# Kernel tuning notes

Measured on AMD Instinct MI355X. Metric: run time of the kernel, lower is better.

The kernel has to match this reference:

```python
import jax, jax.numpy as jnp
import numpy as np

N = 20          # n_qubits
L = 4           # n_layers
B = 4           # batch of states
DIM = 1 << N    # 2^N = 1048576

_H = jnp.asarray((1.0 / np.sqrt(2.0)) * np.array([[1.0, 1.0], [1.0, -1.0]]), dtype=jnp.complex64)


def _apply_1q(psi, U, q):
    # psi: [B, 2^N]; apply 2x2 unitary U on big-endian qubit q
    left = 1 << q
    right = 1 << (N - q - 1)
    out = jnp.einsum('uv,blvr->blur', U, psi.reshape(-1, left, 2, right))
    return out.reshape(-1, DIM)


def _apply_cnot(psi, control, target):
    ctrl_mask = np.uint32(1 << (N - 1 - control))
    targ_mask = np.uint32(1 << (N - 1 - target))
    idx = jnp.arange(DIM, dtype=jnp.uint32)
    perm = jnp.where((idx & ctrl_mask) != 0, idx ^ targ_mask, idx)
    return psi[:, perm]


def _rot_x(theta):
    c = jnp.cos(theta / 2.0).astype(jnp.complex64)
    s = (-1j * jnp.sin(theta / 2.0)).astype(jnp.complex64)
    return jnp.stack([jnp.stack([c, s]), jnp.stack([s, c])])


def _rot_z(theta):
    e = jnp.exp(-0.5j * theta.astype(jnp.complex64))
    z = jnp.zeros((), jnp.complex64)
    return jnp.stack([jnp.stack([e, z]), jnp.stack([z, jnp.conj(e)])])


def _circuit(psi, thetas_x, thetas_z):
    for q in range(N):
        psi = _apply_1q(psi, _H, q)
    for l in range(L):
        for q in range(N):
            psi = _apply_1q(psi, _rot_z(thetas_z[l, q]), q)
        for q in range(N):
            psi = _apply_1q(psi, _rot_x(thetas_x[l, q]), q)
        for q in range(N - 1):  # linear entanglement
            psi = _apply_cnot(psi, q, q + 1)
    return psi


def setup_inputs() -> dict:
    key = jax.random.key(0)
    k1, k2, k3, k4 = jax.random.split(key, 4)
    return {
        'psi0_real': jax.random.normal(k1, (B, DIM), dtype=jnp.float32),
        'psi0_imag': jax.random.normal(k2, (B, DIM), dtype=jnp.float32),
        'thetas_x': jax.random.normal(k3, (L, N), dtype=jnp.float32),
        'thetas_z': jax.random.normal(k4, (L, N), dtype=jnp.float32),
    }


def reference(psi0_real, psi0_imag, thetas_x, thetas_z):
    psi = (psi0_real + 1j * psi0_imag).astype(jnp.complex64)
    return _circuit(psi, thetas_x, thetas_z)
```

## Files before the change

kernel.cpp:

```cpp
#include <hip/hip_runtime.h>
#include <math.h>


#define NQ 20

struct U2 { float r00,i00,r01,i01,r10,i10,r11,i11; };

typedef unsigned int u32x4 __attribute__((ext_vector_type(4)));
typedef float        f32x4 __attribute__((ext_vector_type(4)));

__device__ __forceinline__ uint4 ld_nt4(const uint4* p) {
  u32x4 v = __builtin_nontemporal_load((const u32x4*)p);
  uint4 r; r.x = v[0]; r.y = v[1]; r.z = v[2]; r.w = v[3]; return r;
}
__device__ __forceinline__ void st_nt4(uint4* p, uint4 v) {
  u32x4 t; t[0] = v.x; t[1] = v.y; t[2] = v.z; t[3] = v.w;
  __builtin_nontemporal_store(t, (u32x4*)p);
}
__device__ __forceinline__ float4 ldf_nt4(const float* p) {
  f32x4 v = __builtin_nontemporal_load((const f32x4*)p);
  return make_float4(v[0], v[1], v[2], v[3]);
}
__device__ __forceinline__ void stf_nt4(float* p, float4 v) {
  f32x4 t; t[0] = v.x; t[1] = v.y; t[2] = v.z; t[3] = v.w;
  __builtin_nontemporal_store(t, (f32x4*)p);
}

__device__ __forceinline__ U2 make_u(const float* __restrict__ thx,
                                     const float* __restrict__ thz,
                                     int layer, int q, int withH) {
  float tx = 0.5f * thx[layer*NQ + q];
  float tz = 0.5f * thz[layer*NQ + q];
  float sx, cxv; __sincosf(tx, &sx, &cxv);
  float sz, cz;  __sincosf(tz, &sz, &cz);
  U2 u;
  u.r00 =  cxv*cz;  u.i00 = -cxv*sz;
  u.r01 =  sx*sz;   u.i01 = -sx*cz;
  u.r10 = -sx*sz;   u.i10 = -sx*cz;
  u.r11 =  cxv*cz;  u.i11 =  cxv*sz;
  if (withH) {
    const float r = 0.70710678118654752f;
    float a, b;
    a=u.r00; b=u.r01; u.r00=(a+b)*r; u.r01=(a-b)*r;
    a=u.i00; b=u.i01; u.i00=(a+b)*r; u.i01=(a-b)*r;
    a=u.r10; b=u.r11; u.r10=(a+b)*r; u.r11=(a-b)*r;
    a=u.i10; b=u.i11; u.i10=(a+b)*r; u.i11=(a-b)*r;
  }
  return u;
}

template <int ST>
__device__ __forceinline__ void bfly16(float* re, float* im, const U2 u) {
#pragma unroll
  for (int s = 0; s < 16; ++s) {
    if ((s & ST) == 0) {
      const int s1 = s + ST;
      float ar = re[s], ai = im[s], br = re[s1], bi = im[s1];
      re[s]  = u.r00*ar - u.i00*ai + u.r01*br - u.i01*bi;
      im[s]  = u.r00*ai + u.i00*ar + u.r01*bi + u.i01*br;
      re[s1] = u.r10*ar - u.i10*ai + u.r11*br - u.i11*bi;
      im[s1] = u.r10*ai + u.i10*ar + u.r11*bi + u.i11*br;
    }
  }
}

template <int ST>
__device__ __forceinline__ void bfly16_rx(float* re, float* im, float c, float s) {
#pragma unroll
  for (int k = 0; k < 16; ++k) {
    if ((k & ST) == 0) {
      const int k1 = k + ST;
      float ar = re[k], ai = im[k], br = re[k1], bi = im[k1];
      re[k]  = c*ar + s*bi;
      im[k]  = c*ai - s*br;
      re[k1] = c*br + s*ai;
      im[k1] = c*bi - s*ar;
    }
  }
}

template <int RXONLY, int ST>
__device__ __forceinline__ void gate16(float* re, float* im,
                                       const float* __restrict__ thx,
                                       const float* __restrict__ thz,
                                       int layer, int q, int withH) {
  if (RXONLY) {
    float sx, cx; __sincosf(0.5f * thx[layer*NQ + q], &sx, &cx);
    bfly16_rx<ST>(re, im, cx, sx);
  } else {
    bfly16<ST>(re, im, make_u(thx, thz, layer, q, withH));
  }
}

__device__ __forceinline__ int K(int j) { return j ^ (((j >> 6) & 0xF) << 2); }

__device__ __forceinline__ unsigned pkbf(float a, float b) {
  unsigned r;
  asm("v_cvt_pk_bf16_f32 %0, %1, %2" : "=v"(r) : "v"(a), "v"(b));
  return r;
}
__device__ __forceinline__ float blo(unsigned p) { return __uint_as_float(p << 16); }
__device__ __forceinline__ float bhi(unsigned p) { return __uint_as_float(p & 0xFFFF0000u); }

__device__ __forceinline__ void unpack_g(uint4 v, float* re, float* im) {
  re[0]=blo(v.x); re[1]=bhi(v.x); re[2]=blo(v.y); re[3]=bhi(v.y);
  im[0]=blo(v.z); im[1]=bhi(v.z); im[2]=blo(v.w); im[3]=bhi(v.w);
}

template <int FIN, int RXONLY, int PP>
__global__ __launch_bounds__(256, 5) void pass_a(
    const uint4* __restrict__ src, uint4* __restrict__ dst,
    float* __restrict__ outre,
    const float* __restrict__ thx, const float* __restrict__ thz,
    int layer, int withH) {
  __shared__ __align__(16) float sre[4096];
  __shared__ __align__(16) float sim[4096];
  float4* sre4 = (float4*)sre;
  float4* sim4 = (float4*)sim;
  const int t = threadIdx.x;
  const int b = blockIdx.x >> 8;
  const int m = blockIdx.x & 255;
  const size_t base = (((size_t)b) << NQ) | ((size_t)m << 12);
  float re[16], im[16];

#pragma unroll
  for (int hi = 0; hi < 4; ++hi) {
    const int o = (hi << 10) | (t << 2);
    unpack_g(ld_nt4(src + ((base + o) >> 2)), re + 4*hi, im + 4*hi);
  }
  gate16<RXONLY,1>(re, im, thx, thz, layer, 19, withH);
  gate16<RXONLY,2>(re, im, thx, thz, layer, 18, withH);
  gate16<RXONLY,4>(re, im, thx, thz, layer,  9, withH);
  gate16<RXONLY,8>(re, im, thx, thz, layer,  8, withH);

#pragma unroll
  for (int hi = 0; hi < 4; ++hi) {
    int F = K((hi << 10) | (t << 2)) >> 2;
    sre4[F] = make_float4(re[4*hi+0], re[4*hi+1], re[4*hi+2], re[4*hi+3]);
    sim4[F] = make_float4(im[4*hi+0], im[4*hi+1], im[4*hi+2], im[4*hi+3]);
  }
  __syncthreads();

  const int jt2 = (t & 3) | ((t & 0xFC) << 4);
#pragma unroll
  for (int s = 0; s < 16; ++s) {
    int k = K(jt2 | (s << 2));
    re[s] = sre[k]; im[s] = sim[k];
  }
  gate16<RXONLY,1>(re, im, thx, thz, layer, 17, withH);
  gate16<RXONLY,2>(re, im, thx, thz, layer, 16, withH);
  gate16<RXONLY,4>(re, im, thx, thz, layer, 15, withH);
  gate16<RXONLY,8>(re, im, thx, thz, layer, 14, withH);
#pragma unroll
  for (int s = 0; s < 16; ++s) {
    int k = K(jt2 | (s << 2));
    sre[k] = re[s]; sim[k] = im[s];
  }
  __syncthreads();

  const int jt3 = (t & 63) | ((t & 0xC0) << 4);
#pragma unroll
  for (int s = 0; s < 16; ++s) {
    int k = K(jt3 | (s << 6));
    re[s] = sre[k]; im[s] = sim[k];
  }
  gate16<RXONLY,1>(re, im, thx, thz, layer, 13, withH);
  gate16<RXONLY,2>(re, im, thx, thz, layer, 12, withH);
  gate16<RXONLY,4>(re, im, thx, thz, layer, 11, withH);
  gate16<RXONLY,8>(re, im, thx, thz, layer, 10, withH);
#pragma unroll
  for (int s = 0; s < 16; ++s) {
    int k = K(jt3 | (s << 6));
    sre[k] = re[s]; sim[k] = im[s];
  }
  __syncthreads();

  const int c11 = (m & 1) << 11;
#pragma unroll
  for (int hi = 0; hi < 4; ++hi) {
    int y0 = (hi << 10) | (t << 2);
    int x0 = y0 ^ ((y0 >> 1) & 0x7FF) ^ c11;
    int FG = K(x0 & ~3) >> 2;
    float4 vr = sre4[FG], vi = sim4[FG];
    if (x0 & 2) {
      vr = make_float4(vr.z, vr.w, vr.x, vr.y);
      vi = make_float4(vi.z, vi.w, vi.x, vi.y);
    }
    if (FIN) {
      stf_nt4(outre + base + y0, make_float4(vr.x, vr.y, vr.w, vr.z));
    } else {
      uint4 v;
      v.x = pkbf(vr.x, vr.y); v.y = pkbf(vr.w, vr.z);
      v.z = pkbf(vi.x, vi.y); v.w = pkbf(vi.w, vi.z);
      size_t n;
      if (PP) {
        n = (((size_t)b) << NQ) | ((size_t)m << 4)
          | (size_t)((y0 & 15) | ((y0 >> 4) << 12));
      } else {
        n = base + y0;
      }
      st_nt4(dst + (n >> 2), v);
    }
  }
}

template <int INIT, int DIAG, int PP>
__global__ __launch_bounds__(256, 5) void pass_b(
    const float* __restrict__ in_re, const float* __restrict__ in_im,
    const uint4* __restrict__ src, uint4* __restrict__ dst,
    const float* __restrict__ thx, const float* __restrict__ thz,
    int layer, int withH) {
  __shared__ __align__(16) float sre[4096];
  __shared__ __align__(16) float sim[4096];
  float4* sre4 = (float4*)sre;
  float4* sim4 = (float4*)sim;
  const int t = threadIdx.x;
  const int b = blockIdx.x >> 8;
  const int m = blockIdx.x & 255;
  const size_t base = ((size_t)b) << NQ;
  float re[16], im[16];

  float pb = 0.f, dhi1 = 0.f, dhi2 = 0.f, de1 = 0.f, de2 = 0.f;
  if (DIAG) {
    const float* Z = thz + layer*NQ;
    float s0 = 0.f;
#pragma unroll
    for (int q = 0; q < NQ; ++q) s0 += Z[q];
    pb = -0.5f * s0;
#pragma unroll
    for (int k = 0; k < 8; ++k)
      pb += (m & (1 << k)) ? Z[15 - k] : 0.f;
    pb += (t & 1) ? Z[17] : 0.f;
    pb += (t & 2) ? Z[16] : 0.f;
#pragma unroll
    for (int k = 2; k < 8; ++k)
      pb += (t & (1 << k)) ? Z[9 - k] : 0.f;
    dhi1 = Z[1];  dhi2 = Z[0];
    de1  = Z[19]; de2  = Z[18];
  }
  const float dhi[4] = {0.f, dhi1, dhi2, dhi1 + dhi2};
  const float de[4]  = {0.f, de1,  de2,  de1 + de2};

#pragma unroll
  for (int hi = 0; hi < 4; ++hi) {
    int j0q = (hi << 10) | (t << 2);
    if (INIT) {
      int g0 = ((j0q >> 4) << 12) | (m << 4) | (j0q & 15);
      float4 vr = ldf_nt4(in_re + base + g0);
      float4 vi = ldf_nt4(in_im + base + g0);
      re[4*hi+0]=vr.x; re[4*hi+1]=vr.y; re[4*hi+2]=vr.z; re[4*hi+3]=vr.w;
      im[4*hi+0]=vi.x; im[4*hi+1]=vi.y; im[4*hi+2]=vi.z; im[4*hi+3]=vi.w;
    } else if (PP) {
      size_t nB = base | ((size_t)m << 12) | (size_t)j0q;
      unpack_g(ld_nt4(src + (nB >> 2)), re + 4*hi, im + 4*hi);
    } else {
      int g0 = ((j0q >> 4) << 12) | (m << 4) | (j0q & 15);
      unpack_g(ld_nt4(src + ((base + g0) >> 2)), re + 4*hi, im + 4*hi);
    }
    if (DIAG) {
      float bh = pb + dhi[hi];
#pragma unroll
      for (int e = 0; e < 4; ++e) {
        float sn, cs; __sincosf(bh + de[e], &sn, &cs);
        float r0 = re[4*hi+e], i0 = im[4*hi+e];
        re[4*hi+e] = cs*r0 - sn*i0;
        im[4*hi+e] = cs*i0 + sn*r0;
      }
    }
  }
  gate16<DIAG,4>(re, im, thx, thz, layer, 1, withH);
  gate16<DIAG,8>(re, im, thx, thz, layer, 0, withH);

#pragma unroll
  for (int hi = 0; hi < 4; ++hi) {
    int F = K((hi << 10) | (t << 2)) >> 2;
    sre4[F] = make_float4(re[4*hi+0], re[4*hi+1], re[4*hi+2], re[4*hi+3]);
    sim4[F] = make_float4(im[4*hi+0], im[4*hi+1], im[4*hi+2], im[4*hi+3]);
  }
  __syncthreads();

  const int jt2 = (t & 15) | ((t & 0xF0) << 4);
#pragma unroll
  for (int s = 0; s < 16; ++s) {
    int k = K(jt2 | (s << 4));
    re[s] = sre[k]; im[s] = sim[k];
  }
  gate16<DIAG,1>(re, im, thx, thz, layer, 7, withH);
  gate16<DIAG,2>(re, im, thx, thz, layer, 6, withH);
  gate16<DIAG,4>(re, im, thx, thz, layer, 5, withH);
  gate16<DIAG,8>(re, im, thx, thz, layer, 4, withH);
#pragma unroll
  for (int s = 0; s < 16; ++s) {
    int k = K(jt2 | (s << 4));
    sre[k] = re[s]; sim[k] = im[s];
  }
  __syncthreads();

  const int jt3 = ((t & 63) << 2) | ((t & 0xC0) << 4);
#pragma unroll
  for (int sh = 0; sh < 4; ++sh) {
    int FG = K(jt3 | (sh << 8)) >> 2;
    float4 vr = sre4[FG], vi = sim4[FG];
    re[4*sh+0]=vr.x; re[4*sh+1]=vr.y; re[4*sh+2]=vr.z; re[4*sh+3]=vr.w;
    im[4*sh+0]=vi.x; im[4*sh+1]=vi.y; im[4*sh+2]=vi.z; im[4*sh+3]=vi.w;
  }
  gate16<DIAG,4>(re, im, thx, thz, layer, 3, withH);
  gate16<DIAG,8>(re, im, thx, thz, layer, 2, withH);
#pragma unroll
  for (int sh = 0; sh < 4; ++sh) {
    int FG = K(jt3 | (sh << 8)) >> 2;
    sre4[FG] = make_float4(re[4*sh+0], re[4*sh+1], re[4*sh+2], re[4*sh+3]);
    sim4[FG] = make_float4(im[4*sh+0], im[4*sh+1], im[4*sh+2], im[4*sh+3]);
  }
  __syncthreads();

#pragma unroll
  for (int hi = 0; hi < 4; ++hi) {
    int y0 = (hi << 10) | (t << 2);
    int x0 = y0 ^ ((y0 >> 1) & 0x7F0);
    int FG = K(x0) >> 2;
    float4 vr = sre4[FG], vi = sim4[FG];
    int g0 = ((y0 >> 4) << 12) | (m << 4) | (y0 & 15);
    uint4 v;
    v.x = pkbf(vr.x, vr.y); v.y = pkbf(vr.z, vr.w);
    v.z = pkbf(vi.x, vi.y); v.w = pkbf(vi.z, vi.w);
    st_nt4(dst + ((base + g0) >> 2), v);
  }
}

extern "C" void kernel_launch(void* const* d_in, const int* in_sizes, int n_in,
                              void* d_out, int out_size, void* d_ws, size_t ws_size,
                              hipStream_t stream) {
  const float* p_re = (const float*)d_in[0];
  const float* p_im = (const float*)d_in[1];
  const float* thx  = (const float*)d_in[2];
  const float* thz  = (const float*)d_in[3];
  float* outre = (float*)d_out;
  const size_t HALF = (size_t)16 << 20;
  uint4* ws0 = (uint4*)d_ws;
  uint4* ws1 = (uint4*)((char*)d_ws + HALF);

  dim3 grid(1024), blk(256);

  if (ws_size >= 2 * HALF) {
    pass_b<1,0,1><<<grid, blk, 0, stream>>>(p_re, p_im, nullptr, ws0, thx, thz, 0, 1);
    pass_a<0,0,1><<<grid, blk, 0, stream>>>(ws0, ws1, outre, thx, thz, 0, 1);
    for (int l = 1; l < 3; ++l) {
      pass_b<0,1,1><<<grid, blk, 0, stream>>>(nullptr, nullptr, ws1, ws0, thx, thz, l, 0);
      pass_a<0,1,1><<<grid, blk, 0, stream>>>(ws0, ws1, outre, thx, thz, l, 0);
    }
    pass_b<0,1,1><<<grid, blk, 0, stream>>>(nullptr, nullptr, ws1, ws0, thx, thz, 3, 0);
    pass_a<1,1,1><<<grid, blk, 0, stream>>>(ws0, nullptr, outre, thx, thz, 3, 0);
  } else {
    pass_b<1,0,0><<<grid, blk, 0, stream>>>(p_re, p_im, nullptr, ws0, thx, thz, 0, 1);
    pass_a<0,0,0><<<grid, blk, 0, stream>>>(ws0, ws0, outre, thx, thz, 0, 1);
    for (int l = 1; l < 3; ++l) {
      pass_b<0,1,0><<<grid, blk, 0, stream>>>(nullptr, nullptr, ws0, ws0, thx, thz, l, 0);
      pass_a<0,1,0><<<grid, blk, 0, stream>>>(ws0, ws0, outre, thx, thz, l, 0);
    }
    pass_b<0,1,0><<<grid, blk, 0, stream>>>(nullptr, nullptr, ws0, ws0, thx, thz, 3, 0);
    pass_a<1,1,0><<<grid, blk, 0, stream>>>(ws0, nullptr, outre, thx, thz, 3, 0);
  }
}
```

Baseline: 178.8 us.

## Store shared-memory staging as packed bf16 complex pairs and raise occupancy

The separate fp32 real/imag shared arrays are replaced by one array of packed bf16 (re,im) words, which halves LDS per block (32KB to 16KB) and LDS traffic for each transpose stage. Launch bounds go from 5 to 8 blocks per SM to use the freed LDS. The final global store becomes bit shuffles instead of cvt. The cost is extra bf16 rounding at every intermediate shared-memory stage, so accuracy drops, and register pressure rises under the tighter launch bound.

```diff
diff --git a/kernel.cpp b/kernel.cpp
--- a/kernel.cpp
+++ b/kernel.cpp
@@ -107,16 +107,19 @@
   im[0]=blo(v.z); im[1]=bhi(v.z); im[2]=blo(v.w); im[3]=bhi(v.w);
 }
 
+__device__ __forceinline__ unsigned pkpair(float r, float i) { return pkbf(r, i); }
+__device__ __forceinline__ void unpair(unsigned u, float* r, float* i) {
+  *r = blo(u); *i = bhi(u);
+}
+
 template <int FIN, int RXONLY, int PP>
-__global__ __launch_bounds__(256, 5) void pass_a(
+__global__ __launch_bounds__(256, 8) void pass_a(
     const uint4* __restrict__ src, uint4* __restrict__ dst,
     float* __restrict__ outre,
     const float* __restrict__ thx, const float* __restrict__ thz,
     int layer, int withH) {
-  __shared__ __align__(16) float sre[4096];
-  __shared__ __align__(16) float sim[4096];
-  float4* sre4 = (float4*)sre;
-  float4* sim4 = (float4*)sim;
+  __shared__ __align__(16) unsigned spk[4096];
+  uint4* spk4 = (uint4*)spk;
   const int t = threadIdx.x;
   const int b = blockIdx.x >> 8;
   const int m = blockIdx.x & 255;
@@ -136,16 +139,17 @@
 #pragma unroll
   for (int hi = 0; hi < 4; ++hi) {
     int F = K((hi << 10) | (t << 2)) >> 2;
-    sre4[F] = make_float4(re[4*hi+0], re[4*hi+1], re[4*hi+2], re[4*hi+3]);
-    sim4[F] = make_float4(im[4*hi+0], im[4*hi+1], im[4*hi+2], im[4*hi+3]);
+    spk4[F] = make_uint4(pkpair(re[4*hi+0], im[4*hi+0]),
+                         pkpair(re[4*hi+1], im[4*hi+1]),
+                         pkpair(re[4*hi+2], im[4*hi+2]),
+                         pkpair(re[4*hi+3], im[4*hi+3]));
   }
   __syncthreads();
 
   const int jt2 = (t & 3) | ((t & 0xFC) << 4);
 #pragma unroll
   for (int s = 0; s < 16; ++s) {
-    int k = K(jt2 | (s << 2));
-    re[s] = sre[k]; im[s] = sim[k];
+    unpair(spk[K(jt2 | (s << 2))], re + s, im + s);
   }
   gate16<RXONLY,1>(re, im, thx, thz, layer, 17, withH);
   gate16<RXONLY,2>(re, im, thx, thz, layer, 16, withH);
@@ -153,16 +157,14 @@
   gate16<RXONLY,8>(re, im, thx, thz, layer, 14, withH);
 #pragma unroll
   for (int s = 0; s < 16; ++s) {
-    int k = K(jt2 | (s << 2));
-    sre[k] = re[s]; sim[k] = im[s];
+    spk[K(jt2 | (s << 2))] = pkpair(re[s], im[s]);
   }
   __syncthreads();
 
   const int jt3 = (t & 63) | ((t & 0xC0) << 4);
 #pragma unroll
   for (int s = 0; s < 16; ++s) {
-    int k = K(jt3 | (s << 6));
-    re[s] = sre[k]; im[s] = sim[k];
+    unpair(spk[K(jt3 | (s << 6))], re + s, im + s);
   }
   gate16<RXONLY,1>(re, im, thx, thz, layer, 13, withH);
   gate16<RXONLY,2>(re, im, thx, thz, layer, 12, withH);
@@ -170,8 +172,7 @@
   gate16<RXONLY,8>(re, im, thx, thz, layer, 10, withH);
 #pragma unroll
   for (int s = 0; s < 16; ++s) {
-    int k = K(jt3 | (s << 6));
-    sre[k] = re[s]; sim[k] = im[s];
+    spk[K(jt3 | (s << 6))] = pkpair(re[s], im[s]);
   }
   __syncthreads();
 
@@ -181,17 +182,17 @@
     int y0 = (hi << 10) | (t << 2);
     int x0 = y0 ^ ((y0 >> 1) & 0x7FF) ^ c11;
     int FG = K(x0 & ~3) >> 2;
-    float4 vr = sre4[FG], vi = sim4[FG];
-    if (x0 & 2) {
-      vr = make_float4(vr.z, vr.w, vr.x, vr.y);
-      vi = make_float4(vi.z, vi.w, vi.x, vi.y);
-    }
+    uint4 q = spk4[FG];
+    if (x0 & 2) q = make_uint4(q.z, q.w, q.x, q.y);
     if (FIN) {
-      stf_nt4(outre + base + y0, make_float4(vr.x, vr.y, vr.w, vr.z));
+      stf_nt4(outre + base + y0,
+              make_float4(blo(q.x), blo(q.y), blo(q.w), blo(q.z)));
     } else {
       uint4 v;
-      v.x = pkbf(vr.x, vr.y); v.y = pkbf(vr.w, vr.z);
-      v.z = pkbf(vi.x, vi.y); v.w = pkbf(vi.w, vi.z);
+      v.x = (q.x & 0xFFFFu) | (q.y << 16);
+      v.y = (q.w & 0xFFFFu) | (q.z << 16);
+      v.z = (q.x >> 16) | (q.y & 0xFFFF0000u);
+      v.w = (q.w >> 16) | (q.z & 0xFFFF0000u);
       size_t n;
       if (PP) {
         n = (((size_t)b) << NQ) | ((size_t)m << 4)
@@ -205,15 +206,13 @@
 }
 
 template <int INIT, int DIAG, int PP>
-__global__ __launch_bounds__(256, 5) void pass_b(
+__global__ __launch_bounds__(256, 8) void pass_b(
     const float* __restrict__ in_re, const float* __restrict__ in_im,
     const uint4* __restrict__ src, uint4* __restrict__ dst,
     const float* __restrict__ thx, const float* __restrict__ thz,
     int layer, int withH) {
-  __shared__ __align__(16) float sre[4096];
-  __shared__ __align__(16) float sim[4096];
-  float4* sre4 = (float4*)sre;
-  float4* sim4 = (float4*)sim;
+  __shared__ __align__(16) unsigned spk[4096];
+  uint4* spk4 = (uint4*)spk;
   const int t = threadIdx.x;
   const int b = blockIdx.x >> 8;
   const int m = blockIdx.x & 255;
@@ -274,16 +273,17 @@
 #pragma unroll
   for (int hi = 0; hi < 4; ++hi) {
     int F = K((hi << 10) | (t << 2)) >> 2;
-    sre4[F] = make_float4(re[4*hi+0], re[4*hi+1], re[4*hi+2], re[4*hi+3]);
-    sim4[F] = make_float4(im[4*hi+0], im[4*hi+1], im[4*hi+2], im[4*hi+3]);
+    spk4[F] = make_uint4(pkpair(re[4*hi+0], im[4*hi+0]),
+                         pkpair(re[4*hi+1], im[4*hi+1]),
+                         pkpair(re[4*hi+2], im[4*hi+2]),
+                         pkpair(re[4*hi+3], im[4*hi+3]));
   }
   __syncthreads();
 
   const int jt2 = (t & 15) | ((t & 0xF0) << 4);
 #pragma unroll
   for (int s = 0; s < 16; ++s) {
-    int k = K(jt2 | (s << 4));
-    re[s] = sre[k]; im[s] = sim[k];
+    unpair(spk[K(jt2 | (s << 4))], re + s, im + s);
   }
   gate16<DIAG,1>(re, im, thx, thz, layer, 7, withH);
   gate16<DIAG,2>(re, im, thx, thz, layer, 6, withH);
@@ -291,8 +291,7 @@
   gate16<DIAG,8>(re, im, thx, thz, layer, 4, withH);
 #pragma unroll
   for (int s = 0; s < 16; ++s) {
-    int k = K(jt2 | (s << 4));
-    sre[k] = re[s]; sim[k] = im[s];
+    spk[K(jt2 | (s << 4))] = pkpair(re[s], im[s]);
   }
   __syncthreads();
 
@@ -300,17 +299,21 @@
 #pragma unroll
   for (int sh = 0; sh < 4; ++sh) {
     int FG = K(jt3 | (sh << 8)) >> 2;
-    float4 vr = sre4[FG], vi = sim4[FG];
-    re[4*sh+0]=vr.x; re[4*sh+1]=vr.y; re[4*sh+2]=vr.z; re[4*sh+3]=vr.w;
-    im[4*sh+0]=vi.x; im[4*sh+1]=vi.y; im[4*sh+2]=vi.z; im[4*sh+3]=vi.w;
+    uint4 q = spk4[FG];
+    unpair(q.x, re + 4*sh + 0, im + 4*sh + 0);
+    unpair(q.y, re + 4*sh + 1, im + 4*sh + 1);
+    unpair(q.z, re + 4*sh + 2, im + 4*sh + 2);
+    unpair(q.w, re + 4*sh + 3, im + 4*sh + 3);
   }
   gate16<DIAG,4>(re, im, thx, thz, layer, 3, withH);
   gate16<DIAG,8>(re, im, thx, thz, layer, 2, withH);
 #pragma unroll
   for (int sh = 0; sh < 4; ++sh) {
     int FG = K(jt3 | (sh << 8)) >> 2;
-    sre4[FG] = make_float4(re[4*sh+0], re[4*sh+1], re[4*sh+2], re[4*sh+3]);
-    sim4[FG] = make_float4(im[4*sh+0], im[4*sh+1], im[4*sh+2], im[4*sh+3]);
+    spk4[FG] = make_uint4(pkpair(re[4*sh+0], im[4*sh+0]),
+                          pkpair(re[4*sh+1], im[4*sh+1]),
+                          pkpair(re[4*sh+2], im[4*sh+2]),
+                          pkpair(re[4*sh+3], im[4*sh+3]));
   }
   __syncthreads();
 
@@ -319,11 +322,13 @@
     int y0 = (hi << 10) | (t << 2);
     int x0 = y0 ^ ((y0 >> 1) & 0x7F0);
     int FG = K(x0) >> 2;
-    float4 vr = sre4[FG], vi = sim4[FG];
+    uint4 q = spk4[FG];
     int g0 = ((y0 >> 4) << 12) | (m << 4) | (y0 & 15);
     uint4 v;
-    v.x = pkbf(vr.x, vr.y); v.y = pkbf(vr.z, vr.w);
-    v.z = pkbf(vi.x, vi.y); v.w = pkbf(vi.z, vi.w);
+    v.x = (q.x & 0xFFFFu) | (q.y << 16);
+    v.y = (q.z & 0xFFFFu) | (q.w << 16);
+    v.z = (q.x >> 16) | (q.y & 0xFFFF0000u);
+    v.w = (q.z >> 16) | (q.w & 0xFFFF0000u);
     st_nt4(dst + ((base + g0) >> 2), v);
   }
 }
```

New measurement: 202.4 us. 1.13x slower.
